# Kernel optimization log

Measured on AMD Instinct MI355X. Metric: run time of the kernel, lower is better.

Reference implementation:

```python
import jax, jax.numpy as jnp
import numpy as np

N_HEADS = 8
N_POINTS = 4
SPATIAL = np.array([[64, 64], [32, 32], [16, 16], [8, 8]], dtype=np.int32)


def setup_inputs() -> dict:
    key = jax.random.key(0)
    ks = jax.random.split(key, 12)
    d = 256
    H, L, P, N = N_HEADS, SPATIAL.shape[0], N_POINTS, 8
    lens = SPATIAL[:, 0] * SPATIAL[:, 1]
    Lin = int(lens.sum())
    Lq = Lin
    query = jax.random.normal(ks[0], (N, Lq, d), jnp.float32)
    reference_points = jax.random.uniform(ks[1], (N, Lq, L, 2), jnp.float32)
    input_flatten = jax.random.normal(ks[2], (N, Lin, d), jnp.float32)
    input_spatial_shapes = jnp.asarray(SPATIAL)
    starts = np.concatenate([[0], np.cumsum(lens)[:-1]]).astype(np.int32)
    input_level_start_index = jnp.asarray(starts)
    s = 1.0 / np.sqrt(d)
    W_off = jax.random.normal(ks[3], (H * L * P * 2, d), jnp.float32) * 0.01
    b_off = jax.random.normal(ks[4], (H * L * P * 2,), jnp.float32) * 0.5
    W_attn = jax.random.normal(ks[5], (H * L * P, d), jnp.float32) * 0.02
    b_attn = jnp.zeros((H * L * P,), jnp.float32)
    W_val = jax.random.normal(ks[6], (d, d), jnp.float32) * s
    b_val = jnp.zeros((d,), jnp.float32)
    W_out = jax.random.normal(ks[7], (d, d), jnp.float32) * s
    b_out = jnp.zeros((d,), jnp.float32)
    return {
        'query': query, 'reference_points': reference_points,
        'input_flatten': input_flatten,
        'input_spatial_shapes': input_spatial_shapes,
        'input_level_start_index': input_level_start_index,
        'W_off': W_off, 'b_off': b_off, 'W_attn': W_attn, 'b_attn': b_attn,
        'W_val': W_val, 'b_val': b_val, 'W_out': W_out, 'b_out': b_out,
    }


def _bilinear(img, Hl, Wl, x, y):
    # img: [B, Ch, Hl*Wl]; x, y: [B, Q, P] pixel coords (align_corners=False)
    # zero padding mode: out-of-range corners contribute 0
    x0 = jnp.floor(x)
    y0 = jnp.floor(y)
    wx = x - x0
    wy = y - y0

    def gather(xi, yi):
        valid = (xi >= 0) & (xi <= Wl - 1) & (yi >= 0) & (yi <= Hl - 1)
        ii = jnp.clip(xi, 0, Wl - 1).astype(jnp.int32)
        jj = jnp.clip(yi, 0, Hl - 1).astype(jnp.int32)
        idx = jj * Wl + ii  # [B, Q, P]
        B, Q, P = idx.shape
        v = jnp.take_along_axis(img, idx.reshape(B, 1, Q * P), axis=2)
        v = v.reshape(B, img.shape[1], Q, P)
        return v * valid[:, None].astype(img.dtype)

    return (gather(x0, y0) * ((1 - wx) * (1 - wy))[:, None]
            + gather(x0 + 1, y0) * (wx * (1 - wy))[:, None]
            + gather(x0, y0 + 1) * ((1 - wx) * wy)[:, None]
            + gather(x0 + 1, y0 + 1) * (wx * wy)[:, None])


def reference(query, reference_points, input_flatten, input_spatial_shapes,
              input_level_start_index, W_off, b_off, W_attn, b_attn,
              W_val, b_val, W_out, b_out):
    shapes = np.asarray(input_spatial_shapes)  # static structural metadata
    N, Lq, d = query.shape
    Lin = input_flatten.shape[1]
    L = shapes.shape[0]
    H, P = N_HEADS, N_POINTS
    Ch = d // H

    value = input_flatten @ W_val.T + b_val                       # [N, Lin, d]
    value = value.reshape(N, Lin, H, Ch).transpose(0, 2, 3, 1)    # [N, H, Ch, Lin]
    value = value.reshape(N * H, Ch, Lin)

    off = (query @ W_off.T + b_off).reshape(N, Lq, H, L, P, 2)
    attn = (query @ W_attn.T + b_attn).reshape(N, Lq, H, L * P)
    attn = jax.nn.softmax(attn, axis=-1).reshape(N, Lq, H, L, P)

    # normalizer is (W, H) per level
    norm = jnp.asarray(np.stack([shapes[:, 1], shapes[:, 0]], -1), query.dtype)
    loc = reference_points[:, :, None, :, None, :] + off / norm[None, None, None, :, None, :]

    attn_p = attn.transpose(0, 2, 1, 3, 4).reshape(N * H, Lq, L, P)
    starts = np.concatenate([[0], np.cumsum(shapes[:, 0] * shapes[:, 1])])

    out = jnp.zeros((N * H, Ch, Lq), query.dtype)
    for l in range(L):
        Hl, Wl = int(shapes[l, 0]), int(shapes[l, 1])
        v_l = value[:, :, starts[l]:starts[l + 1]]                # [B, Ch, Hl*Wl]
        g = loc[:, :, :, l].transpose(0, 2, 1, 3, 4).reshape(N * H, Lq, P, 2)
        # grid_sample align_corners=False with grid=2*loc-1 -> pixel = loc*W - 0.5
        x = g[..., 0] * Wl - 0.5
        y = g[..., 1] * Hl - 0.5
        samp = _bilinear(v_l, Hl, Wl, x, y)                       # [B, Ch, Lq, P]
        out = out + jnp.einsum('bcqp,bqp->bcq', samp, attn_p[:, :, l])

    out = out.reshape(N, H, Ch, Lq).transpose(0, 3, 1, 2).reshape(N, Lq, d)
    return out @ W_out.T + b_out
```

## Files before the change

kernel.cpp:

```cpp
#include <hip/hip_runtime.h>
#include <hip/hip_bf16.h>
#include <hip/hip_fp16.h>

#define NQ   5440
#define NB   8
#define DIM  256
#define NH   8
#define CHN  32
#define NLV  4
#define NPT  4
#define MTOT (NB * NQ)

typedef __attribute__((ext_vector_type(8))) short s16x8;
typedef __attribute__((ext_vector_type(4))) float f32x4;
typedef unsigned short ushort_t;

#define WVAL 0
#define WOFF 65536
#define WATT 131072
#define WOUT 163840
#define WTOT 229376

__device__ __forceinline__ short f2bf(float x) {
    union { __hip_bfloat16 b; short s; } u;
    u.b = __float2bfloat16(x);
    return u.s;
}

__device__ __forceinline__ void gload_lds16(const void* g, void* l) {
    __builtin_amdgcn_global_load_lds(
        (const __attribute__((address_space(1))) unsigned int*)g,
        (__attribute__((address_space(3))) unsigned int*)l, 16, 0, 0);
}

__device__ __forceinline__ void cvt8b(const float* s, ushort_t* d) {
    f32x4 a = *(const f32x4*)s, b = *(const f32x4*)(s + 4);
    s16x8 v;
#pragma unroll
    for (int e = 0; e < 4; ++e) { v[e] = f2bf(a[e]); v[e + 4] = f2bf(b[e]); }
    *(s16x8*)d = v;
}

__global__ __launch_bounds__(256) void cvt_weights(const float* __restrict__ wv,
                                                   const float* __restrict__ wo,
                                                   const float* __restrict__ wa,
                                                   const float* __restrict__ wu,
                                                   ushort_t* __restrict__ wb) {
    const int i = (blockIdx.x * 256 + threadIdx.x) * 8;
    if (i >= WTOT) return;
    const float* src;
    int off;
    if (i < WOFF)      { src = wv; off = WVAL; }
    else if (i < WATT) { src = wo; off = WOFF; }
    else if (i < WOUT) { src = wa; off = WATT; }
    else               { src = wu; off = WOUT; }
    cvt8b(src + (i - off), wb + i);
}

__device__ __forceinline__ void stC(float* p, float v) { *p = v; }
__device__ __forceinline__ void stC(__half* p, float v) { *p = __float2half(v); }
__device__ __forceinline__ void stC(ushort_t* p, float v) { *(short*)p = f2bf(v); }

template <typename AT, typename CT>
__device__ __forceinline__ void gemm_core(const AT* __restrict__ A,
                                          const ushort_t* __restrict__ Wt,
                                          const float* __restrict__ biasT,
                                          CT* __restrict__ Ct, int ldC, int rowBase) {
    __shared__ ushort_t As[128 * 64];
    __shared__ ushort_t Ws[128 * 64];

    const int t = threadIdx.x;
    const int lane = t & 63, w = t >> 6;
    const int wm = w >> 1, wn = w & 1;
    const int lr = lane & 15, quad = lane >> 4;

    f32x4 acc[4][4];
#pragma unroll
    for (int i = 0; i < 4; ++i)
#pragma unroll
        for (int j = 0; j < 4; ++j)
#pragma unroll
            for (int r = 0; r < 4; ++r) acc[i][j][r] = 0.f;

    for (int ks = 0; ks < 4; ++ks) {
        if (ks) __syncthreads();
#pragma unroll
        for (int i = 0; i < 4; ++i) {
            const int c = t + i * 256;
            const int r = c >> 3, s = c & 7;
            const int g = (s - r) & 7;
            const int ke = ks * 64 + g * 8;
            gload_lds16(Wt + (size_t)r * DIM + ke,
                        &Ws[(size_t)(i * 256 + w * 64) * 8]);
            if constexpr (sizeof(AT) == 2) {
                gload_lds16(A + (size_t)(rowBase + r) * DIM + ke,
                            &As[(size_t)(i * 256 + w * 64) * 8]);
            } else {
                const float* pa = (const float*)A + (size_t)(rowBase + r) * DIM + ke;
                f32x4 a0 = *(const f32x4*)pa, a1 = *(const f32x4*)(pa + 4);
                s16x8 av;
#pragma unroll
                for (int e = 0; e < 4; ++e) {
                    av[e] = f2bf(a0[e]);
                    av[e + 4] = f2bf(a1[e]);
                }
                *(s16x8*)&As[(size_t)c * 8] = av;
            }
        }
        __syncthreads();
#pragma unroll
        for (int kk = 0; kk < 64; kk += 32) {
            s16x8 afr[4], wfr[4];
            const int G = (kk >> 3) + quad;
#pragma unroll
            for (int i = 0; i < 4; ++i) {
                const int R = wm * 64 + i * 16 + lr;
                afr[i] = *(const s16x8*)&As[(R * 8 + ((G + R) & 7)) * 8];
            }
#pragma unroll
            for (int j = 0; j < 4; ++j) {
                const int R = wn * 64 + j * 16 + lr;
                wfr[j] = *(const s16x8*)&Ws[(R * 8 + ((G + R) & 7)) * 8];
            }
#pragma unroll
            for (int i = 0; i < 4; ++i)
#pragma unroll
                for (int j = 0; j < 4; ++j)
                    acc[i][j] = __builtin_amdgcn_mfma_f32_16x16x32_bf16(
                        afr[i], wfr[j], acc[i][j], 0, 0, 0);
        }
    }

    float bj[4];
#pragma unroll
    for (int j = 0; j < 4; ++j) bj[j] = biasT[wn * 64 + j * 16 + lr];
#pragma unroll
    for (int i = 0; i < 4; ++i)
#pragma unroll
        for (int r = 0; r < 4; ++r) {
            int row = rowBase + wm * 64 + i * 16 + quad * 4 + r;
#pragma unroll
            for (int j = 0; j < 4; ++j) {
                int col = wn * 64 + j * 16 + lr;
                stC(&Ct[(size_t)row * ldC + col], acc[i][j][r] + bj[j]);
            }
        }
}

__global__ __launch_bounds__(256) void gemm_fused(const float* __restrict__ inputf,
                                                  const float* __restrict__ query,
                                                  const ushort_t* __restrict__ wb,
                                                  const float* __restrict__ b_val,
                                                  const float* __restrict__ b_off,
                                                  const float* __restrict__ b_attn,
                                                  __half* __restrict__ bval,
                                                  __half* __restrict__ v_off,
                                                  __half* __restrict__ v_attn) {
    const int gy = blockIdx.y;
    const int rowBase = blockIdx.x * 128;
    if (gy < 2)
        gemm_core<float, __half>(inputf, wb + WVAL + (size_t)gy * 128 * DIM,
                                 b_val + gy * 128, bval + gy * 128, DIM, rowBase);
    else if (gy < 4)
        gemm_core<float, __half>(query, wb + WOFF + (size_t)(gy - 2) * 128 * DIM,
                                 b_off + (gy - 2) * 128, v_off + (gy - 2) * 128, DIM,
                                 rowBase);
    else
        gemm_core<float, __half>(query, wb + WATT, b_attn, v_attn, 128, rowBase);
}

__global__ __launch_bounds__(256) void gemm_out(const ushort_t* __restrict__ A,
                                                const ushort_t* __restrict__ wb,
                                                const float* __restrict__ bias,
                                                float* __restrict__ C) {
    gemm_core<ushort_t, float>(A, wb + WOUT + (size_t)blockIdx.y * 128 * DIM,
                               bias + blockIdx.y * 128, C + blockIdx.y * 128, DIM,
                               blockIdx.x * 128);
}

__global__ __launch_bounds__(128) void sample_kernel(
    const float* __restrict__ refp,
    const __half* __restrict__ off,
    const __half* __restrict__ attn,
    const __half* __restrict__ bval,
    const int* __restrict__ shapes,
    const int* __restrict__ starts,
    ushort_t* __restrict__ sampb)
{
    const int n = blockIdx.x & 7;
    const int qBase = n * NQ + (blockIdx.x >> 3) * 4;
    const int t = threadIdx.x;

    __shared__ __align__(16) int     sidx[512][4];
    __shared__ __align__(16) __half2 sww[512][4];

#pragma unroll
    for (int it = 0; it < 4; ++it) {
        const int i = t + it * 128;
        const int q4 = i >> 7, hlp = i & 127;
        const int h = hlp >> 4, lp = hlp & 15, l = lp >> 2;
        const int q = qBase + q4;
        const int Wl = shapes[2 * l + 1], Hl = shapes[2 * l];
        const float Wf = (float)Wl, Hf = (float)Hl;
        const float2 rp = *(const float2*)(refp + ((size_t)q * NLV + l) * 2);
        const __half2 oo2 = ((const __half2*)off)[(size_t)q * 128 + h * 16 + lp];
        const float2 oo = __half22float2(oo2);
        const float x = (rp.x + oo.x / Wf) * Wf - 0.5f;
        const float y = (rp.y + oo.y / Hf) * Hf - 0.5f;

        float logit = __half2float(attn[(size_t)q * 128 + h * 16 + lp]);
        float m = logit;
#pragma unroll
        for (int s = 8; s >= 1; s >>= 1) m = fmaxf(m, __shfl_xor(m, s, 16));
        float e = __expf(logit - m);
        float ss = e;
#pragma unroll
        for (int s = 8; s >= 1; s >>= 1) ss += __shfl_xor(ss, s, 16);
        const float aw = e / ss;

        const float xf = floorf(x), yf = floorf(y);
        const int ix = (int)xf, iy = (int)yf;
        const float wx = x - xf, wy = y - yf;
        const int ix1 = ix + 1, iy1 = iy + 1;
        const bool bx0 = (ix >= 0) & (ix < Wl);
        const bool bx1 = (ix1 >= 0) & (ix1 < Wl);
        const bool by0 = (iy >= 0) & (iy < Hl);
        const bool by1 = (iy1 >= 0) & (iy1 < Hl);
        const int cx0 = min(max(ix, 0), Wl - 1), cx1 = min(max(ix1, 0), Wl - 1);
        const int cy0 = min(max(iy, 0), Hl - 1), cy1 = min(max(iy1, 0), Hl - 1);
        const int base = n * NQ + starts[l];
        int4 id;
        id.x = (base + cy0 * Wl + cx0) << 9;
        id.y = (base + cy0 * Wl + cx1) << 9;
        id.z = (base + cy1 * Wl + cx0) << 9;
        id.w = (base + cy1 * Wl + cx1) << 9;
        __half2 wp[4];
        wp[0] = __float2half2_rn((bx0 && by0) ? aw * (1.f - wx) * (1.f - wy) : 0.f);
        wp[1] = __float2half2_rn((bx1 && by0) ? aw * wx * (1.f - wy) : 0.f);
        wp[2] = __float2half2_rn((bx0 && by1) ? aw * (1.f - wx) * wy : 0.f);
        wp[3] = __float2half2_rn((bx1 && by1) ? aw * wx * wy : 0.f);
        *(int4*)sidx[i] = id;
        *(uint4*)&sww[i][0] = *(uint4*)wp;
    }
    __syncthreads();

    const int q4 = t >> 5, r = t & 31;
    const int h = r >> 2, cg = r & 3;
    const int q = qBase + q4;
    const char* vb = (const char*)bval + h * 64 + cg * 16;

    __half2 acch[4];
    float accf[8];
#pragma unroll
    for (int e = 0; e < 4; ++e) acch[e] = __float2half2_rn(0.f);
#pragma unroll
    for (int e = 0; e < 8; ++e) accf[e] = 0.f;

#pragma unroll
    for (int j = 0; j < 16; ++j) {
        const int lp = (j + h) & 15;
        const int slot = (q4 << 7) + (h << 4) + lp;
        const int4 id = *(const int4*)sidx[slot];
        uint4 wu = *(const uint4*)&sww[slot][0];
        const __half2* wp = (const __half2*)&wu;
        int idc[4] = {id.x, id.y, id.z, id.w};
#pragma unroll
        for (int c = 0; c < 4; ++c) {
            const uint4 u = *(const uint4*)(vb + (size_t)(unsigned)idc[c]);
            const __half2* hv = (const __half2*)&u;
#pragma unroll
            for (int e = 0; e < 4; ++e) acch[e] = __hfma2(hv[e], wp[c], acch[e]);
        }
        if ((j & 3) == 3) {
#pragma unroll
            for (int e = 0; e < 4; ++e) {
                float2 f = __half22float2(acch[e]);
                accf[2 * e] += f.x;
                accf[2 * e + 1] += f.y;
                acch[e] = __float2half2_rn(0.f);
            }
        }
    }

    s16x8 o;
#pragma unroll
    for (int e = 0; e < 8; ++e) o[e] = f2bf(accf[e]);
    *(s16x8*)(sampb + (size_t)q * DIM + h * CHN + cg * 8) = o;
}

extern "C" void kernel_launch(void* const* d_in, const int* in_sizes, int n_in,
                              void* d_out, int out_size, void* d_ws, size_t ws_size,
                              hipStream_t stream) {
    const float* query  = (const float*)d_in[0];
    const float* refp   = (const float*)d_in[1];
    const float* inputf = (const float*)d_in[2];
    const int* shapes   = (const int*)d_in[3];
    const int* starts   = (const int*)d_in[4];
    const float* W_off  = (const float*)d_in[5];
    const float* b_off  = (const float*)d_in[6];
    const float* W_attn = (const float*)d_in[7];
    const float* b_attn = (const float*)d_in[8];
    const float* W_val  = (const float*)d_in[9];
    const float* b_val  = (const float*)d_in[10];
    const float* W_out  = (const float*)d_in[11];
    const float* b_out  = (const float*)d_in[12];
    float* out = (float*)d_out;

    const size_t AB = (size_t)MTOT * DIM * 2;
    char* ws = (char*)d_ws;
    ushort_t* wb     = (ushort_t*)ws;
    __half*   bval   = (__half*)(ws + 512 * 1024);
    __half*   v_off  = (__half*)(ws + 512 * 1024 + AB);
    __half*   v_attn = (__half*)(ws + 512 * 1024 + 2 * AB);
    ushort_t* sampb  = (ushort_t*)(ws + 512 * 1024 + 2 * AB + AB / 2);

    cvt_weights<<<dim3(WTOT / 2048), dim3(256), 0, stream>>>(W_val, W_off, W_attn,
                                                             W_out, wb);
    gemm_fused<<<dim3(MTOT / 128, 5), dim3(256), 0, stream>>>(
        inputf, query, wb, b_val, b_off, b_attn, bval, v_off, v_attn);
    sample_kernel<<<dim3(MTOT / 4), dim3(128), 0, stream>>>(
        refp, v_off, v_attn, bval, shapes, starts, sampb);
    gemm_out<<<dim3(MTOT / 128, 2), dim3(256), 0, stream>>>(sampb, wb, b_out, out);
}
```

Measured before the change: 257.3 us.

## Store value projection head-major and prefetch next sampling point's gathers

The value GEMM now writes its output head-split, as [head][batch*query][32 channels] in fp16. Each head's bilinear corner gathers therefore hit a compact 64-byte-per-pixel plane, and neighbouring pixels share cache lines instead of being 512 bytes apart. The sampling loop is also software-pipelined: it loads the indices, weights and four corner vectors for the next point before doing the FMAs on the current one. This hides gather latency at the cost of more live registers, and the last iteration issues one redundant prefetch.

```diff
diff --git a/kernel.cpp b/kernel.cpp
--- a/kernel.cpp
+++ b/kernel.cpp
@@ -61,11 +61,12 @@
 __device__ __forceinline__ void stC(__half* p, float v) { *p = __float2half(v); }
 __device__ __forceinline__ void stC(ushort_t* p, float v) { *(short*)p = f2bf(v); }
 
-template <typename AT, typename CT>
+template <typename AT, typename CT, bool HSPLIT>
 __device__ __forceinline__ void gemm_core(const AT* __restrict__ A,
                                           const ushort_t* __restrict__ Wt,
                                           const float* __restrict__ biasT,
-                                          CT* __restrict__ Ct, int ldC, int rowBase) {
+                                          CT* __restrict__ Ct, int ldC, int rowBase,
+                                          int colOff) {
     __shared__ ushort_t As[128 * 64];
     __shared__ ushort_t Ws[128 * 64];
 
@@ -142,7 +143,15 @@
 #pragma unroll
             for (int j = 0; j < 4; ++j) {
                 int col = wn * 64 + j * 16 + lr;
-                stC(&Ct[(size_t)row * ldC + col], acc[i][j][r] + bj[j]);
+                float v = acc[i][j][r] + bj[j];
+                if constexpr (HSPLIT) {
+                    const int gc = colOff + col;
+                    const size_t addr =
+                        ((size_t)(gc >> 5) * MTOT + row) * CHN + (gc & 31);
+                    stC(&Ct[addr], v);
+                } else {
+                    stC(&Ct[(size_t)row * ldC + col], v);
+                }
             }
         }
 }
@@ -159,23 +168,24 @@
     const int gy = blockIdx.y;
     const int rowBase = blockIdx.x * 128;
     if (gy < 2)
-        gemm_core<float, __half>(inputf, wb + WVAL + (size_t)gy * 128 * DIM,
-                                 b_val + gy * 128, bval + gy * 128, DIM, rowBase);
+        gemm_core<float, __half, true>(inputf, wb + WVAL + (size_t)gy * 128 * DIM,
+                                       b_val + gy * 128, bval, 0, rowBase, gy * 128);
     else if (gy < 4)
-        gemm_core<float, __half>(query, wb + WOFF + (size_t)(gy - 2) * 128 * DIM,
-                                 b_off + (gy - 2) * 128, v_off + (gy - 2) * 128, DIM,
-                                 rowBase);
+        gemm_core<float, __half, false>(query, wb + WOFF + (size_t)(gy - 2) * 128 * DIM,
+                                        b_off + (gy - 2) * 128,
+                                        v_off + (gy - 2) * 128, DIM, rowBase, 0);
     else
-        gemm_core<float, __half>(query, wb + WATT, b_attn, v_attn, 128, rowBase);
+        gemm_core<float, __half, false>(query, wb + WATT, b_attn, v_attn, 128,
+                                        rowBase, 0);
 }
 
 __global__ __launch_bounds__(256) void gemm_out(const ushort_t* __restrict__ A,
                                                 const ushort_t* __restrict__ wb,
                                                 const float* __restrict__ bias,
                                                 float* __restrict__ C) {
-    gemm_core<ushort_t, float>(A, wb + WOUT + (size_t)blockIdx.y * 128 * DIM,
-                               bias + blockIdx.y * 128, C + blockIdx.y * 128, DIM,
-                               blockIdx.x * 128);
+    gemm_core<ushort_t, float, false>(A, wb + WOUT + (size_t)blockIdx.y * 128 * DIM,
+                                      bias + blockIdx.y * 128, C + blockIdx.y * 128,
+                                      DIM, blockIdx.x * 128, 0);
 }
 
 __global__ __launch_bounds__(128) void sample_kernel(
@@ -228,12 +238,12 @@
         const bool by1 = (iy1 >= 0) & (iy1 < Hl);
         const int cx0 = min(max(ix, 0), Wl - 1), cx1 = min(max(ix1, 0), Wl - 1);
         const int cy0 = min(max(iy, 0), Hl - 1), cy1 = min(max(iy1, 0), Hl - 1);
-        const int base = n * NQ + starts[l];
+        const int base = starts[l];
         int4 id;
-        id.x = (base + cy0 * Wl + cx0) << 9;
-        id.y = (base + cy0 * Wl + cx1) << 9;
-        id.z = (base + cy1 * Wl + cx0) << 9;
-        id.w = (base + cy1 * Wl + cx1) << 9;
+        id.x = (base + cy0 * Wl + cx0) << 6;
+        id.y = (base + cy0 * Wl + cx1) << 6;
+        id.z = (base + cy1 * Wl + cx0) << 6;
+        id.w = (base + cy1 * Wl + cx1) << 6;
         __half2 wp[4];
         wp[0] = __float2half2_rn((bx0 && by0) ? aw * (1.f - wx) * (1.f - wy) : 0.f);
         wp[1] = __float2half2_rn((bx1 && by0) ? aw * wx * (1.f - wy) : 0.f);
@@ -247,7 +257,9 @@
     const int q4 = t >> 5, r = t & 31;
     const int h = r >> 2, cg = r & 3;
     const int q = qBase + q4;
-    const char* vb = (const char*)bval + h * 64 + cg * 16;
+    const char* vb = (const char*)bval +
+                     (((size_t)h * MTOT + (size_t)n * NQ) << 6) + cg * 16;
+    const int sbase = (q4 << 7) + (h << 4);
 
     __half2 acch[4];
     float accf[8];
@@ -256,20 +268,34 @@
 #pragma unroll
     for (int e = 0; e < 8; ++e) accf[e] = 0.f;
 
+    int4 idA = *(const int4*)sidx[sbase + (h & 15)];
+    uint4 wA = *(const uint4*)&sww[sbase + (h & 15)][0];
+    uint4 uA0 = *(const uint4*)(vb + (unsigned)idA.x);
+    uint4 uA1 = *(const uint4*)(vb + (unsigned)idA.y);
+    uint4 uA2 = *(const uint4*)(vb + (unsigned)idA.z);
+    uint4 uA3 = *(const uint4*)(vb + (unsigned)idA.w);
+
 #pragma unroll
     for (int j = 0; j < 16; ++j) {
-        const int lp = (j + h) & 15;
-        const int slot = (q4 << 7) + (h << 4) + lp;
-        const int4 id = *(const int4*)sidx[slot];
-        uint4 wu = *(const uint4*)&sww[slot][0];
-        const __half2* wp = (const __half2*)&wu;
-        int idc[4] = {id.x, id.y, id.z, id.w};
-#pragma unroll
-        for (int c = 0; c < 4; ++c) {
-            const uint4 u = *(const uint4*)(vb + (size_t)(unsigned)idc[c]);
-            const __half2* hv = (const __half2*)&u;
-#pragma unroll
-            for (int e = 0; e < 4; ++e) acch[e] = __hfma2(hv[e], wp[c], acch[e]);
+        const int lpn = (j + 1 + h) & 15;
+        const int4 idB = *(const int4*)sidx[sbase + lpn];
+        const uint4 wB = *(const uint4*)&sww[sbase + lpn][0];
+        const uint4 uB0 = *(const uint4*)(vb + (unsigned)idB.x);
+        const uint4 uB1 = *(const uint4*)(vb + (unsigned)idB.y);
+        const uint4 uB2 = *(const uint4*)(vb + (unsigned)idB.z);
+        const uint4 uB3 = *(const uint4*)(vb + (unsigned)idB.w);
+
+        const __half2* wp = (const __half2*)&wA;
+        const __half2* h0 = (const __half2*)&uA0;
+        const __half2* h1 = (const __half2*)&uA1;
+        const __half2* h2 = (const __half2*)&uA2;
+        const __half2* h3 = (const __half2*)&uA3;
+#pragma unroll
+        for (int e = 0; e < 4; ++e) {
+            acch[e] = __hfma2(h0[e], wp[0], acch[e]);
+            acch[e] = __hfma2(h1[e], wp[1], acch[e]);
+            acch[e] = __hfma2(h2[e], wp[2], acch[e]);
+            acch[e] = __hfma2(h3[e], wp[3], acch[e]);
         }
         if ((j & 3) == 3) {
 #pragma unroll
@@ -280,6 +306,8 @@
                 acch[e] = __float2half2_rn(0.f);
             }
         }
+        idA = idB; wA = wB;
+        uA0 = uB0; uA1 = uB1; uA2 = uB2; uA3 = uB3;
     }
 
     s16x8 o;
```

Measured after the change: 257.6 us. No clear change (+0.1%).
